# Kernel optimization log

Hardware: AMD Instinct MI355X
Metric: run time of the kernel (lower is better)

## Reference

```python
import jax, jax.numpy as jnp
import numpy as np

BS, H = 2048, 1024
XDIM = 2048 + 4 * 64  # x + R*W = 2304
IN = XDIM + 2 * H     # 4352


def setup_inputs() -> dict:
    key = jax.random.key(0)
    ks = jax.random.split(key, 11)
    s = 1.0 / np.sqrt(IN)  # torch Linear default init scale
    return {
        "input_x": jax.random.normal(ks[0], (BS, XDIM), jnp.float32),
        "previous_time": jax.random.normal(ks[1], (BS, H), jnp.float32),
        "previous_layer": jax.random.normal(ks[2], (BS, H), jnp.float32),
        "old_state": jnp.zeros((BS, H), jnp.float32),
        "Wi": jax.random.normal(ks[3], (H, IN), jnp.float32) * s,
        "bi": jax.random.normal(ks[4], (H,), jnp.float32) * s,
        "Wf": jax.random.normal(ks[5], (H, IN), jnp.float32) * s,
        "bf": jax.random.normal(ks[6], (H,), jnp.float32) * s,
        "Wo": jax.random.normal(ks[7], (H, IN), jnp.float32) * s,
        "bo": jax.random.normal(ks[8], (H,), jnp.float32) * s,
        "Ws": jax.random.normal(ks[9], (H, IN), jnp.float32) * s,
        "bs_state": jax.random.normal(ks[10], (H,), jnp.float32) * s,
    }


def reference(input_x, previous_time, previous_layer, old_state,
              Wi, bi, Wf, bf, Wo, bo, Ws, bs_state):
    # semicolon_input: [bs, x + R*W + 2h]
    z = jnp.concatenate([input_x, previous_time, previous_layer], axis=1)
    # Fuse the four projections into one GEMM: [bs, 4h]
    W_all = jnp.concatenate([Wi, Wf, Wo, Ws], axis=0)          # [4h, IN]
    b_all = jnp.concatenate([bi, bf, bo, bs_state], axis=0)    # [4h]
    proj = z @ W_all.T + b_all
    gi, gf, go, gs = jnp.split(proj, 4, axis=1)
    input_gate = jax.nn.sigmoid(gi)
    forget_gate = jax.nn.sigmoid(gf)
    output_gate = jax.nn.sigmoid(go)
    new_state = forget_gate * old_state + input_gate * jnp.tanh(gs)
    new_hidden = output_gate * jnp.tanh(new_state)
    return new_hidden
```

## Files before the change

### kernel.cpp

```cpp
#include <hip/hip_runtime.h>
#include <stdint.h>
#include <stddef.h>

#define M_DIM 2048
#define N_DIM 4096
#define K_DIM 4352
#define H_DIM 1024
#define X_DIM 2304

#define A_OFF 0u
#define B_OFF 17825792u

typedef __bf16 bf16x8 __attribute__((ext_vector_type(8)));
typedef float f32x4 __attribute__((ext_vector_type(4)));

__device__ __forceinline__ unsigned short f32_to_bf16(float f) {
    unsigned u = __float_as_uint(f);
    u += 0x7FFFu + ((u >> 16) & 1u);
    return (unsigned short)(u >> 16);
}

__device__ __forceinline__ float sigm_(float x) { return 1.f / (1.f + __expf(-x)); }
__device__ __forceinline__ float tanh_(float x) {
    x = fminf(15.f, fmaxf(-15.f, x));
    float e = __expf(2.f * x);
    return (e - 1.f) / (e + 1.f);
}

__global__ __launch_bounds__(256) void convert_kernel(
    const float* __restrict__ x, const float* __restrict__ pt,
    const float* __restrict__ pl,
    const float* __restrict__ Wi, const float* __restrict__ Wf,
    const float* __restrict__ Wo, const float* __restrict__ Ws,
    unsigned short* __restrict__ Abf, unsigned short* __restrict__ Bbf)
{
    const int row = blockIdx.x;
    const float* srow = nullptr;
    unsigned short* drow;
    if (row < M_DIM) {
        drow = Abf + (size_t)row * K_DIM;
    } else {
        int n = row - M_DIM;
        int g = n >> 10, h = n & 1023;
        const float* W = (g == 0) ? Wi : (g == 1) ? Wf : (g == 2) ? Wo : Ws;
        srow = W + (size_t)h * K_DIM;
        drow = Bbf + (size_t)(h * 4 + g) * K_DIM;
    }

    for (int c8 = threadIdx.x; c8 < K_DIM / 8; c8 += 256) {
        int col = c8 * 8;
        const float* s;
        if (row < M_DIM) {
            if (col < X_DIM)              s = x  + (size_t)row * X_DIM + col;
            else if (col < X_DIM + H_DIM) s = pt + (size_t)row * H_DIM + (col - X_DIM);
            else                          s = pl + (size_t)row * H_DIM + (col - X_DIM - H_DIM);
        } else {
            s = srow + col;
        }
        float4 v0 = ((const float4*)s)[0];
        float4 v1 = ((const float4*)s)[1];
        union { unsigned short h[8]; uint4 u; } r;
        r.h[0] = f32_to_bf16(v0.x); r.h[1] = f32_to_bf16(v0.y);
        r.h[2] = f32_to_bf16(v0.z); r.h[3] = f32_to_bf16(v0.w);
        r.h[4] = f32_to_bf16(v1.x); r.h[5] = f32_to_bf16(v1.y);
        r.h[6] = f32_to_bf16(v1.z); r.h[7] = f32_to_bf16(v1.w);
        *(uint4*)(drow + col) = r.u;
    }
}

__global__ __launch_bounds__(512, 2) void gemm_fused(
    const unsigned short* __restrict__ A,
    const unsigned short* __restrict__ B,
    const float* __restrict__ old_state,
    const float* __restrict__ bi, const float* __restrict__ bfv,
    const float* __restrict__ bo, const float* __restrict__ bs,
    float* __restrict__ out)
{
    __shared__ __align__(16) char smem[147456];
    float* sP = (float*)smem;

    const int tid  = threadIdx.x;
    const int lane = tid & 63;
    const int wave = tid >> 6;
    const int wm = (wave >> 2) * 64;
    const int wn = (wave & 3) * 64;

    const int b   = blockIdx.x;
    const int xcd = b & 7;
    const int j   = b >> 3;
    const int m0  = (j >> 1) * 128;
    const int n0  = (xcd * 2 + (j & 1)) * 256;

    const int urow = tid >> 3;
    const int ukb  = (tid & 7) ^ ((tid >> 3) & 7);
    const unsigned short* Asrc = A + (size_t)(m0 + urow) * K_DIM + ukb * 8;
    const unsigned short* Bsrc = B + (size_t)(n0 + urow) * K_DIM + ukb * 8;

    const int fr  = lane & 15;
    const int kb0 = lane >> 4;
    const int sw  = fr & 7;
    const int sK0 = ((kb0    ) ^ sw) * 16;
    const int sK1 = ((kb0 ^ 4) ^ sw) * 16;
    const int aRow =         (wm + fr) * 128;
    const int bRow = 16384 + (wn + fr) * 128;

    f32x4 acc[4][4];
#pragma unroll
    for (int i = 0; i < 4; ++i)
#pragma unroll
        for (int jj = 0; jj < 4; ++jj) acc[i][jj] = (f32x4){0.f, 0.f, 0.f, 0.f};

    bf16x8 aF[4], bF[4], bG[4];

#define GLDS(GP, LP) __builtin_amdgcn_global_load_lds(                          \
        (const __attribute__((address_space(1))) unsigned*)(GP),                \
        (__attribute__((address_space(3))) unsigned*)(LP), 16, 0, 0)

    auto STAGE3a = [&](int t, int cs) {
        const size_t ko = (size_t)t * 64;
        char* base = smem + cs * 49152;
        GLDS(Asrc + ko,                     base +             wave * 1024);
        GLDS(Asrc + (size_t)64  * K_DIM + ko, base + 8192    + wave * 1024);
        GLDS(Bsrc + ko,                     base + 16384     + wave * 1024);
    };
    auto STAGE3b = [&](int t, int cs) {
        const size_t ko = (size_t)t * 64;
        char* base = smem + cs * 49152 + 16384;
        GLDS(Bsrc + (size_t)64  * K_DIM + ko, base + 8192  + wave * 1024);
        GLDS(Bsrc + (size_t)128 * K_DIM + ko, base + 16384 + wave * 1024);
        GLDS(Bsrc + (size_t)192 * K_DIM + ko, base + 24576 + wave * 1024);
    };

#define RD_Q0(C) {                                                              \
        const char* bb_ = smem + (C) * 49152;                                   \
        aF[0] = *(const bf16x8*)(bb_ + aRow + 0 * 2048 + sK0);                  \
        aF[1] = *(const bf16x8*)(bb_ + aRow + 1 * 2048 + sK0);                  \
        bF[0] = *(const bf16x8*)(bb_ + bRow + 0 * 2048 + sK0);                  \
        bF[1] = *(const bf16x8*)(bb_ + bRow + 1 * 2048 + sK0); }
#define RD_Q1(C) {                                                              \
        const char* bb_ = smem + (C) * 49152;                                   \
        aF[2] = *(const bf16x8*)(bb_ + aRow + 2 * 2048 + sK0);                  \
        aF[3] = *(const bf16x8*)(bb_ + aRow + 3 * 2048 + sK0);                  \
        bF[2] = *(const bf16x8*)(bb_ + bRow + 2 * 2048 + sK0);                  \
        bF[3] = *(const bf16x8*)(bb_ + bRow + 3 * 2048 + sK0); }
#define RD_Q2(C) {                                                              \
        const char* bb_ = smem + (C) * 49152;                                   \
        aF[0] = *(const bf16x8*)(bb_ + aRow + 0 * 2048 + sK1);                  \
        aF[1] = *(const bf16x8*)(bb_ + aRow + 1 * 2048 + sK1);                  \
        bG[0] = *(const bf16x8*)(bb_ + bRow + 0 * 2048 + sK1);                  \
        bG[1] = *(const bf16x8*)(bb_ + bRow + 1 * 2048 + sK1); }
#define RD_Q3(C) {                                                              \
        const char* bb_ = smem + (C) * 49152;                                   \
        aF[2] = *(const bf16x8*)(bb_ + aRow + 2 * 2048 + sK1);                  \
        aF[3] = *(const bf16x8*)(bb_ + aRow + 3 * 2048 + sK1);                  \
        bG[2] = *(const bf16x8*)(bb_ + bRow + 2 * 2048 + sK1);                  \
        bG[3] = *(const bf16x8*)(bb_ + bRow + 3 * 2048 + sK1); }

#define MM(I0, I1, BB)                                                          \
    _Pragma("unroll")                                                           \
    for (int j_ = 0; j_ < 4; ++j_) {                                            \
        acc[I0][j_] = __builtin_amdgcn_mfma_f32_16x16x32_bf16(                  \
            aF[(I0) & 1 ? 1 : 0 + ((I0) >= 2 ? 2 : 0)], BB[j_], acc[I0][j_], 0, 0, 0); \
        acc[I1][j_] = __builtin_amdgcn_mfma_f32_16x16x32_bf16(                  \
            aF[(I1) & 1 ? ((I1) >= 2 ? 3 : 1) : 2], BB[j_], acc[I1][j_], 0, 0, 0); \
    }
#undef MM
#define MM_Q0                                                                   \
    _Pragma("unroll")                                                           \
    for (int j_ = 0; j_ < 4; ++j_) {                                            \
        acc[0][j_] = __builtin_amdgcn_mfma_f32_16x16x32_bf16(aF[0], bF[j_], acc[0][j_], 0, 0, 0); \
        acc[1][j_] = __builtin_amdgcn_mfma_f32_16x16x32_bf16(aF[1], bF[j_], acc[1][j_], 0, 0, 0); }
#define MM_Q1                                                                   \
    _Pragma("unroll")                                                           \
    for (int j_ = 0; j_ < 4; ++j_) {                                            \
        acc[2][j_] = __builtin_amdgcn_mfma_f32_16x16x32_bf16(aF[2], bF[j_], acc[2][j_], 0, 0, 0); \
        acc[3][j_] = __builtin_amdgcn_mfma_f32_16x16x32_bf16(aF[3], bF[j_], acc[3][j_], 0, 0, 0); }
#define MM_Q2                                                                   \
    _Pragma("unroll")                                                           \
    for (int j_ = 0; j_ < 4; ++j_) {                                            \
        acc[0][j_] = __builtin_amdgcn_mfma_f32_16x16x32_bf16(aF[0], bG[j_], acc[0][j_], 0, 0, 0); \
        acc[1][j_] = __builtin_amdgcn_mfma_f32_16x16x32_bf16(aF[1], bG[j_], acc[1][j_], 0, 0, 0); }
#define MM_Q3                                                                   \
    _Pragma("unroll")                                                           \
    for (int j_ = 0; j_ < 4; ++j_) {                                            \
        acc[2][j_] = __builtin_amdgcn_mfma_f32_16x16x32_bf16(aF[2], bG[j_], acc[2][j_], 0, 0, 0); \
        acc[3][j_] = __builtin_amdgcn_mfma_f32_16x16x32_bf16(aF[3], bG[j_], acc[3][j_], 0, 0, 0); }

#define VM6 asm volatile("s_waitcnt vmcnt(6)" ::: "memory")
#define VM0 asm volatile("s_waitcnt vmcnt(0)" ::: "memory")

#define PH(RDLINE, STLINE, MMLINE, VMLINE)                                      \
    do {                                                                        \
        RDLINE; STLINE;                                                         \
        __builtin_amdgcn_sched_barrier(0);                                      \
        __builtin_amdgcn_s_barrier();                                           \
        __builtin_amdgcn_s_setprio(1);                                          \
        MMLINE;                                                                 \
        __builtin_amdgcn_s_setprio(0);                                          \
        __builtin_amdgcn_sched_barrier(0);                                      \
        VMLINE;                                                                 \
        __builtin_amdgcn_s_barrier();                                           \
    } while (0)

#define TILE(C, CN, CS, T)                                                      \
    PH(RD_Q1(C), STAGE3a((T) + 2, CS), MM_Q0, (void)0);                         \
    PH(RD_Q2(C), STAGE3b((T) + 2, CS), MM_Q1, (void)0);                         \
    PH(RD_Q3(C), (void)0,              MM_Q2, VM6);                             \
    PH(RD_Q0(CN), (void)0,             MM_Q3, (void)0);

    STAGE3a(0, 0); STAGE3b(0, 0);
    STAGE3a(1, 1); STAGE3b(1, 1);
    VM6;
    __builtin_amdgcn_s_barrier();
    RD_Q0(0);

    for (int it = 0; it < 22; ++it) {
        const int t = it * 3;
        TILE(0, 1, 2, t);
        TILE(1, 2, 0, t + 1);
        TILE(2, 0, 1, t + 2);
    }
    PH(RD_Q1(0), (void)0, MM_Q0, (void)0);
    PH(RD_Q2(0), (void)0, MM_Q1, (void)0);
    PH(RD_Q3(0), (void)0, MM_Q2, VM0);
    PH(RD_Q0(1), (void)0, MM_Q3, (void)0);
    PH(RD_Q1(1), (void)0, MM_Q0, (void)0);
    PH(RD_Q2(1), (void)0, MM_Q1, (void)0);
    PH(RD_Q3(1), (void)0, MM_Q2, (void)0);
    __builtin_amdgcn_s_setprio(1);
    MM_Q3;
    __builtin_amdgcn_s_setprio(0);

#undef TILE
#undef PH
#undef VM6
#undef VM0
#undef MM_Q0
#undef MM_Q1
#undef MM_Q2
#undef MM_Q3
#undef RD_Q0
#undef RD_Q1
#undef RD_Q2
#undef RD_Q3
#undef GLDS

    const int cw = lane & 15;
    const int rw = (lane >> 4) * 4;
    const int hl = tid & 15;
    const int rb = tid >> 4;

    for (int p = 0; p < 4; ++p) {
        __syncthreads();
        if ((wave & 3) == p) {
#pragma unroll
            for (int i = 0; i < 4; ++i)
#pragma unroll
                for (int jj = 0; jj < 4; ++jj)
#pragma unroll
                    for (int r = 0; r < 4; ++r)
                        sP[(wm + i * 16 + rw + r) * 76 + jj * 16 + cw] = acc[i][jj][r];
        }
        __syncthreads();

        const int hg = (n0 >> 2) + p * 16 + hl;
        const float b_i = bi[hg], b_f = bfv[hg], b_o = bo[hg], b_s = bs[hg];
#pragma unroll
        for (int k = 0; k < 4; ++k) {
            const int row = rb + 32 * k;
            float4 g = *(const float4*)(sP + row * 76 + hl * 4);
            const size_t oidx = (size_t)(m0 + row) * H_DIM + hg;
            float old = old_state[oidx];
            float ig = sigm_(g.x + b_i);
            float fg = sigm_(g.y + b_f);
            float og = sigm_(g.z + b_o);
            float ts = tanh_(g.w + b_s);
            out[oidx] = og * tanh_(fg * old + ig * ts);
        }
    }
}

extern "C" void kernel_launch(void* const* d_in, const int* in_sizes, int n_in,
                              void* d_out, int out_size, void* d_ws, size_t ws_size,
                              hipStream_t stream) {
    const float* x   = (const float*)d_in[0];
    const float* pt  = (const float*)d_in[1];
    const float* pl  = (const float*)d_in[2];
    const float* old = (const float*)d_in[3];
    const float* Wi  = (const float*)d_in[4];
    const float* bi  = (const float*)d_in[5];
    const float* Wf  = (const float*)d_in[6];
    const float* bf  = (const float*)d_in[7];
    const float* Wo  = (const float*)d_in[8];
    const float* bo  = (const float*)d_in[9];
    const float* Ws  = (const float*)d_in[10];
    const float* bs  = (const float*)d_in[11];
    float* out = (float*)d_out;

    char* ws = (char*)d_ws;
    unsigned short* Abf = (unsigned short*)(ws + A_OFF);
    unsigned short* Bbf = (unsigned short*)(ws + B_OFF);

    convert_kernel<<<M_DIM + N_DIM, 256, 0, stream>>>(x, pt, pl, Wi, Wf, Wo, Ws, Abf, Bbf);

    gemm_fused<<<256, 512, 0, stream>>>(Abf, Bbf, old, bi, bf, bo, bs, out);
}
```

Baseline: 225.9 us.

## Shrink GEMM tile to 128x128 with 4 waves and double-buffered LDS

Replaces the 128x256 tile with 8 waves and a triple-buffered 144KB LDS pipeline by a 128x128 tile with 4 waves, two 32KB LDS buffers and 512 blocks. The loads for the next K-slice are issued before a full vmcnt(0) wait each tile. The aim is more blocks and more resident workgroups per CU to hide latency. In exchange each tile reuses loaded data less, and the full wait in every iteration can expose global-load latency.

```diff
diff --git a/kernel.cpp b/kernel.cpp
--- a/kernel.cpp
+++ b/kernel.cpp
@@ -68,7 +68,7 @@
     }
 }
 
-__global__ __launch_bounds__(512, 2) void gemm_fused(
+__global__ __launch_bounds__(256, 2) void gemm_fused(
     const unsigned short* __restrict__ A,
     const unsigned short* __restrict__ B,
     const float* __restrict__ old_state,
@@ -76,25 +76,25 @@
     const float* __restrict__ bo, const float* __restrict__ bs,
     float* __restrict__ out)
 {
-    __shared__ __align__(16) char smem[147456];
+    __shared__ __align__(16) char smem[65536];
     float* sP = (float*)smem;
 
     const int tid  = threadIdx.x;
     const int lane = tid & 63;
     const int wave = tid >> 6;
-    const int wm = (wave >> 2) * 64;
-    const int wn = (wave & 3) * 64;
+    const int wm = (wave >> 1) * 64;
+    const int wn = (wave & 1) * 64;
 
     const int b   = blockIdx.x;
     const int xcd = b & 7;
     const int j   = b >> 3;
-    const int m0  = (j >> 1) * 128;
-    const int n0  = (xcd * 2 + (j & 1)) * 256;
-
-    const int urow = tid >> 3;
-    const int ukb  = (tid & 7) ^ ((tid >> 3) & 7);
-    const unsigned short* Asrc = A + (size_t)(m0 + urow) * K_DIM + ukb * 8;
-    const unsigned short* Bsrc = B + (size_t)(n0 + urow) * K_DIM + ukb * 8;
+    const int n0  = (xcd * 4 + (j & 3)) * 128;
+    const int m0  = (j >> 2) * 128;
+
+    const int srow = wave * 8 + (lane >> 3);
+    const int c8s  = ((lane & 7) ^ (lane >> 3)) * 8;
+    const unsigned short* Aw = A + (size_t)(m0 + srow) * K_DIM + c8s;
+    const unsigned short* Bw = B + (size_t)(n0 + srow) * K_DIM + c8s;
 
     const int fr  = lane & 15;
     const int kb0 = lane >> 4;
@@ -116,55 +116,44 @@
         (const __attribute__((address_space(1))) unsigned*)(GP),                \
         (__attribute__((address_space(3))) unsigned*)(LP), 16, 0, 0)
 
-    auto STAGE3a = [&](int t, int cs) {
-        const size_t ko = (size_t)t * 64;
-        char* base = smem + cs * 49152;
-        GLDS(Asrc + ko,                     base +             wave * 1024);
-        GLDS(Asrc + (size_t)64  * K_DIM + ko, base + 8192    + wave * 1024);
-        GLDS(Bsrc + ko,                     base + 16384     + wave * 1024);
+    auto STAGE_A = [&](int kt, int bufOff) {
+#pragma unroll
+        for (int i = 0; i < 4; ++i)
+            GLDS(Aw + (size_t)i * 32 * K_DIM + kt,
+                 smem + bufOff + i * 4096 + wave * 1024);
     };
-    auto STAGE3b = [&](int t, int cs) {
-        const size_t ko = (size_t)t * 64;
-        char* base = smem + cs * 49152 + 16384;
-        GLDS(Bsrc + (size_t)64  * K_DIM + ko, base + 8192  + wave * 1024);
-        GLDS(Bsrc + (size_t)128 * K_DIM + ko, base + 16384 + wave * 1024);
-        GLDS(Bsrc + (size_t)192 * K_DIM + ko, base + 24576 + wave * 1024);
+    auto STAGE_B = [&](int kt, int bufOff) {
+#pragma unroll
+        for (int i = 0; i < 4; ++i)
+            GLDS(Bw + (size_t)i * 32 * K_DIM + kt,
+                 smem + bufOff + 16384 + i * 4096 + wave * 1024);
     };
 
-#define RD_Q0(C) {                                                              \
-        const char* bb_ = smem + (C) * 49152;                                   \
+#define RD_Q0(BUF) {                                                            \
+        const char* bb_ = smem + (BUF);                                         \
         aF[0] = *(const bf16x8*)(bb_ + aRow + 0 * 2048 + sK0);                  \
         aF[1] = *(const bf16x8*)(bb_ + aRow + 1 * 2048 + sK0);                  \
         bF[0] = *(const bf16x8*)(bb_ + bRow + 0 * 2048 + sK0);                  \
         bF[1] = *(const bf16x8*)(bb_ + bRow + 1 * 2048 + sK0); }
-#define RD_Q1(C) {                                                              \
-        const char* bb_ = smem + (C) * 49152;                                   \
+#define RD_Q1(BUF) {                                                            \
+        const char* bb_ = smem + (BUF);                                         \
         aF[2] = *(const bf16x8*)(bb_ + aRow + 2 * 2048 + sK0);                  \
         aF[3] = *(const bf16x8*)(bb_ + aRow + 3 * 2048 + sK0);                  \
         bF[2] = *(const bf16x8*)(bb_ + bRow + 2 * 2048 + sK0);                  \
         bF[3] = *(const bf16x8*)(bb_ + bRow + 3 * 2048 + sK0); }
-#define RD_Q2(C) {                                                              \
-        const char* bb_ = smem + (C) * 49152;                                   \
+#define RD_Q2(BUF) {                                                            \
+        const char* bb_ = smem + (BUF);                                         \
         aF[0] = *(const bf16x8*)(bb_ + aRow + 0 * 2048 + sK1);                  \
         aF[1] = *(const bf16x8*)(bb_ + aRow + 1 * 2048 + sK1);                  \
         bG[0] = *(const bf16x8*)(bb_ + bRow + 0 * 2048 + sK1);                  \
         bG[1] = *(const bf16x8*)(bb_ + bRow + 1 * 2048 + sK1); }
-#define RD_Q3(C) {                                                              \
-        const char* bb_ = smem + (C) * 49152;                                   \
+#define RD_Q3(BUF) {                                                            \
+        const char* bb_ = smem + (BUF);                                         \
         aF[2] = *(const bf16x8*)(bb_ + aRow + 2 * 2048 + sK1);                  \
         aF[3] = *(const bf16x8*)(bb_ + aRow + 3 * 2048 + sK1);                  \
         bG[2] = *(const bf16x8*)(bb_ + bRow + 2 * 2048 + sK1);                  \
         bG[3] = *(const bf16x8*)(bb_ + bRow + 3 * 2048 + sK1); }
 
-#define MM(I0, I1, BB)                                                          \
-    _Pragma("unroll")                                                           \
-    for (int j_ = 0; j_ < 4; ++j_) {                                            \
-        acc[I0][j_] = __builtin_amdgcn_mfma_f32_16x16x32_bf16(                  \
-            aF[(I0) & 1 ? 1 : 0 + ((I0) >= 2 ? 2 : 0)], BB[j_], acc[I0][j_], 0, 0, 0); \
-        acc[I1][j_] = __builtin_amdgcn_mfma_f32_16x16x32_bf16(                  \
-            aF[(I1) & 1 ? ((I1) >= 2 ? 3 : 1) : 2], BB[j_], acc[I1][j_], 0, 0, 0); \
-    }
-#undef MM
 #define MM_Q0                                                                   \
     _Pragma("unroll")                                                           \
     for (int j_ = 0; j_ < 4; ++j_) {                                            \
@@ -186,10 +175,9 @@
         acc[2][j_] = __builtin_amdgcn_mfma_f32_16x16x32_bf16(aF[2], bG[j_], acc[2][j_], 0, 0, 0); \
         acc[3][j_] = __builtin_amdgcn_mfma_f32_16x16x32_bf16(aF[3], bG[j_], acc[3][j_], 0, 0, 0); }
 
-#define VM6 asm volatile("s_waitcnt vmcnt(6)" ::: "memory")
 #define VM0 asm volatile("s_waitcnt vmcnt(0)" ::: "memory")
 
-#define PH(RDLINE, STLINE, MMLINE, VMLINE)                                      \
+#define PH(RDLINE, STLINE, MMLINE)                                              \
     do {                                                                        \
         RDLINE; STLINE;                                                         \
         __builtin_amdgcn_sched_barrier(0);                                      \
@@ -197,43 +185,36 @@
         __builtin_amdgcn_s_setprio(1);                                          \
         MMLINE;                                                                 \
         __builtin_amdgcn_s_setprio(0);                                          \
+    } while (0)
+
+#define TILE(CB, CNB, KTN, DOST, DORD)                                          \
+    PH(RD_Q1(CB), if (DOST) STAGE_A((KTN), (CNB)), MM_Q0);                      \
+    PH(RD_Q2(CB), if (DOST) STAGE_B((KTN), (CNB)), MM_Q1);                      \
+    PH(RD_Q3(CB), (void)0,                         MM_Q2);                      \
+    do {                                                                        \
+        if (DOST) VM0;                                                          \
         __builtin_amdgcn_sched_barrier(0);                                      \
-        VMLINE;                                                                 \
         __builtin_amdgcn_s_barrier();                                           \
-    } while (0)
-
-#define TILE(C, CN, CS, T)                                                      \
-    PH(RD_Q1(C), STAGE3a((T) + 2, CS), MM_Q0, (void)0);                         \
-    PH(RD_Q2(C), STAGE3b((T) + 2, CS), MM_Q1, (void)0);                         \
-    PH(RD_Q3(C), (void)0,              MM_Q2, VM6);                             \
-    PH(RD_Q0(CN), (void)0,             MM_Q3, (void)0);
-
-    STAGE3a(0, 0); STAGE3b(0, 0);
-    STAGE3a(1, 1); STAGE3b(1, 1);
-    VM6;
+        if (DORD) RD_Q0(CNB);                                                   \
+        __builtin_amdgcn_s_setprio(1);                                          \
+        MM_Q3;                                                                  \
+        __builtin_amdgcn_s_setprio(0);                                          \
+    } while (0);
+
+    STAGE_A(0, 0); STAGE_B(0, 0);
+    VM0;
     __builtin_amdgcn_s_barrier();
     RD_Q0(0);
 
-    for (int it = 0; it < 22; ++it) {
-        const int t = it * 3;
-        TILE(0, 1, 2, t);
-        TILE(1, 2, 0, t + 1);
-        TILE(2, 0, 1, t + 2);
-    }
-    PH(RD_Q1(0), (void)0, MM_Q0, (void)0);
-    PH(RD_Q2(0), (void)0, MM_Q1, (void)0);
-    PH(RD_Q3(0), (void)0, MM_Q2, VM0);
-    PH(RD_Q0(1), (void)0, MM_Q3, (void)0);
-    PH(RD_Q1(1), (void)0, MM_Q0, (void)0);
-    PH(RD_Q2(1), (void)0, MM_Q1, (void)0);
-    PH(RD_Q3(1), (void)0, MM_Q2, (void)0);
-    __builtin_amdgcn_s_setprio(1);
-    MM_Q3;
-    __builtin_amdgcn_s_setprio(0);
+    for (int kt = 0; kt < 4224; kt += 128) {
+        TILE(0,     32768, kt + 64,  true, true);
+        TILE(32768, 0,     kt + 128, true, true);
+    }
+    TILE(0,     32768, 4288, true,  true);
+    TILE(32768, 0,     0,    false, false);
 
 #undef TILE
 #undef PH
-#undef VM6
 #undef VM0
 #undef MM_Q0
 #undef MM_Q1
@@ -250,9 +231,9 @@
     const int hl = tid & 15;
     const int rb = tid >> 4;
 
-    for (int p = 0; p < 4; ++p) {
+    for (int p = 0; p < 2; ++p) {
         __syncthreads();
-        if ((wave & 3) == p) {
+        if ((wave & 1) == p) {
 #pragma unroll
             for (int i = 0; i < 4; ++i)
 #pragma unroll
@@ -266,8 +247,8 @@
         const int hg = (n0 >> 2) + p * 16 + hl;
         const float b_i = bi[hg], b_f = bfv[hg], b_o = bo[hg], b_s = bs[hg];
 #pragma unroll
-        for (int k = 0; k < 4; ++k) {
-            const int row = rb + 32 * k;
+        for (int k = 0; k < 8; ++k) {
+            const int row = rb + 16 * k;
             float4 g = *(const float4*)(sP + row * 76 + hl * 4);
             const size_t oidx = (size_t)(m0 + row) * H_DIM + hg;
             float old = old_state[oidx];
@@ -303,5 +284,5 @@
 
     convert_kernel<<<M_DIM + N_DIM, 256, 0, stream>>>(x, pt, pl, Wi, Wf, Wo, Ws, Abf, Bbf);
 
-    gemm_fused<<<256, 512, 0, stream>>>(Abf, Bbf, old, bi, bf, bo, bs, out);
-}
+    gemm_fused<<<512, 256, 0, stream>>>(Abf, Bbf, old, bi, bf, bo, bs, out);
+}
```

Measured after the change: 222.4 us. No clear change (-1.5%).
